# Kernel optimization log

Hardware: AMD Instinct MI355X
Metric: run time of the kernel (lower is better)

The kernel has to match this reference:

```python
import jax, jax.numpy as jnp
import numpy as np

DIM = 768
N_HEADS = 12
HEAD_DIM = DIM // N_HEADS
SCALE = HEAD_DIM ** -0.5


def setup_inputs() -> dict:
    key = jax.random.key(0)
    ks = jax.random.split(key, 5)
    x = jax.random.normal(ks[0], (8, 1024, DIM), dtype=jnp.float32)
    w_qkv = jax.random.normal(ks[1], (DIM, 3 * DIM), dtype=jnp.float32) * (DIM ** -0.5)
    b_qkv = jnp.zeros((3 * DIM,), dtype=jnp.float32)
    w_proj = jax.random.normal(ks[2], (DIM, DIM), dtype=jnp.float32) * (DIM ** -0.5)
    b_proj = jnp.zeros((DIM,), dtype=jnp.float32)
    return {"x": x, "w_qkv": w_qkv, "b_qkv": b_qkv, "w_proj": w_proj, "b_proj": b_proj}


def reference(x, w_qkv, b_qkv, w_proj, b_proj):
    B, N, _ = x.shape
    qkv = x @ w_qkv + b_qkv                       # [B, N, 3*DIM]
    qkv = qkv.reshape(B, N, 3, N_HEADS, HEAD_DIM)
    q = qkv[:, :, 0].transpose(0, 2, 1, 3)        # [B, H, N, D]
    k = qkv[:, :, 1].transpose(0, 2, 1, 3)
    v = qkv[:, :, 2].transpose(0, 2, 1, 3)
    attn = jnp.einsum('bhnd,bhmd->bhnm', q, k) * SCALE
    attn = jax.nn.softmax(attn, axis=-1)
    out = jnp.einsum('bhnm,bhmd->bhnd', attn, v)  # [B, H, N, D]
    out = out.transpose(0, 2, 1, 3).reshape(B, N, DIM)
    return out @ w_proj + b_proj
```

## Files before the change

kernel.cpp:

```cpp
#include <hip/hip_runtime.h>
#include <hip/hip_bf16.h>

#define NHEADS 12
#define HDIM   64
#define SEQ    1024
#define NBATCH 8
#define MODELD 768
#define QKVD   2304
#define BHEADS (NBATCH * NHEADS)

typedef __attribute__((ext_vector_type(8))) short          bf16x8;
typedef __attribute__((ext_vector_type(8))) unsigned short u16x8;
typedef __attribute__((ext_vector_type(4))) unsigned short u16x4;
typedef __attribute__((ext_vector_type(4))) float          f32x4;

static __device__ __forceinline__ unsigned short f2bf(float f) {
  unsigned int u = __float_as_uint(f);
  u += 0x7fffu + ((u >> 16) & 1u);
  return (unsigned short)(u >> 16);
}

static __device__ __forceinline__ unsigned int pk2(float x, float y) {
  __hip_bfloat162 h = __float22bfloat162_rn(make_float2(x, y));
  return *(unsigned int*)&h;
}

static __device__ __forceinline__ void gld_lds16(const void* g, void* l) {
  __builtin_amdgcn_global_load_lds((const __attribute__((address_space(1))) void*)g,
                                   (__attribute__((address_space(3))) void*)l, 16, 0, 0);
}

#define QSC 0.18033688f

static __device__ __forceinline__ void transpose_body(
    const float* __restrict__ in, unsigned short* __restrict__ out,
    int R, int C, int bx, int by, int tid) {
  __shared__ float t[32][33];
  const int c0 = bx * 32, r0 = by * 32;
  const int lr = tid >> 3;
  const int lc = (tid & 7) * 4;
  const float* p = in + (size_t)(r0 + lr) * C + c0 + lc;
  float4 v = *(const float4*)p;
  t[lr][lc]     = v.x;
  t[lr][lc + 1] = v.y;
  t[lr][lc + 2] = v.z;
  t[lr][lc + 3] = v.w;
  __syncthreads();
  unsigned short* q = out + (size_t)(c0 + lr) * R + r0 + lc;
  q[0] = f2bf(t[lc][lr]);
  q[1] = f2bf(t[lc + 1][lr]);
  q[2] = f2bf(t[lc + 2][lr]);
  q[3] = f2bf(t[lc + 3][lr]);
}

__global__ __launch_bounds__(256) void prep(
    const float* __restrict__ x, unsigned short* __restrict__ Xb,
    const float* __restrict__ w_qkv, unsigned short* __restrict__ wqkvT,
    const float* __restrict__ w_proj, unsigned short* __restrict__ wprojT) {
  const int id = blockIdx.x;
  const int tid = threadIdx.x;
  if (id < 3072) {
    const int i = (id * 256 + tid) * 8;
    const float4 a0 = *(const float4*)(x + i);
    const float4 a1 = *(const float4*)(x + i + 4);
    union { unsigned int u[4]; u16x8 v; } w;
    w.u[0] = pk2(a0.x, a0.y); w.u[1] = pk2(a0.z, a0.w);
    w.u[2] = pk2(a1.x, a1.y); w.u[3] = pk2(a1.z, a1.w);
    *(u16x8*)(Xb + i) = w.v;
  } else if (id < 4800) {
    const int u = id - 3072;
    transpose_body(w_qkv, wqkvT, MODELD, QKVD, u % 72, u / 72, tid);
  } else {
    const int u = id - 4800;
    transpose_body(w_proj, wprojT, MODELD, MODELD, u % 24, u / 24, tid);
  }
}

#define GEMM_CORE(AP, BP)                                                      \
  const int tid  = threadIdx.x;                                                \
  const int lane = tid & 63;                                                   \
  const int wave = tid >> 6;                                                   \
  const int wm = wave >> 1, wn = wave & 1;                                     \
  const int fr = lane & 15;                                                    \
  const int fq = lane >> 4;                                                    \
  const int swz = (fr & 7) << 4;                                               \
  const int srow8 = lane >> 3;                                                 \
  const int scb8 = (((lane & 7) ^ srow8) << 4);                                \
  f32x4 acc[4][4] = {};                                                        \
  auto stA = [&](int dbuf, int kb, int R) {                                    \
    gld_lds16(AP + (size_t)(R + srow8) * 1536 + kb + scb8,                     \
              (char*)smem + dbuf * 16384 + R * 128);                           \
  };                                                                           \
  auto stB = [&](int dbuf, int kb, int R) {                                    \
    gld_lds16(BP + (size_t)(R + srow8) * 1536 + kb + scb8,                     \
              (char*)smem + 32768 + dbuf * 16384 + R * 128);                   \
  };                                                                           \
  _Pragma("unroll")                                                            \
  for (int pt = 0; pt < 2; ++pt) {                                             \
    const int kb = pt * 128;                                                   \
    stA(pt, kb, wave * 8);      stA(pt, kb, 32 + wave * 8);                    \
    stA(pt, kb, 64 + wave * 8); stA(pt, kb, 96 + wave * 8);                    \
    stB(pt, kb, wave * 8);      stB(pt, kb, 64 + wave * 8);                    \
    stB(pt, kb, 32 + wave * 8); stB(pt, kb, 96 + wave * 8);                    \
  }                                                                            \
  asm volatile("s_waitcnt vmcnt(8)" ::: "memory");                             \
  __builtin_amdgcn_s_barrier();                                                \
  for (int kt = 0; kt < 12; ++kt) {                                            \
    const int db = kt & 1;                                                     \
    const char* Ad = (const char*)smem + db * 16384;                           \
    const char* Bd = (const char*)smem + 32768 + db * 16384;                   \
    bf16x8 a[4][2], b[4][2];                                                   \
                                                        \
    _Pragma("unroll")                                                          \
    for (int i = 0; i < 4; ++i)                                                \
      _Pragma("unroll")                                                        \
      for (int c = 0; c < 2; ++c)                                              \
        a[i][c] = *(const bf16x8*)(Ad + (wm * 64 + i * 16 + fr) * 128 +        \
                                   ((c * 64 + fq * 16) ^ swz));                \
    _Pragma("unroll")                                                          \
    for (int j = 0; j < 2; ++j)                                                \
      _Pragma("unroll")                                                        \
      for (int c = 0; c < 2; ++c)                                              \
        b[j][c] = *(const bf16x8*)(Bd + (wn * 64 + j * 16 + fr) * 128 +        \
                                   ((c * 64 + fq * 16) ^ swz));                \
    if (kt >= 1 && kt <= 10) {                   \
      stB(db ^ 1, (kt + 1) * 128, 32 + wave * 8);                              \
      stB(db ^ 1, (kt + 1) * 128, 96 + wave * 8);                              \
    }                                                                          \
    if (kt < 11) asm volatile("s_waitcnt vmcnt(8)" ::: "memory");              \
    else         asm volatile("s_waitcnt vmcnt(0)" ::: "memory");              \
    __builtin_amdgcn_s_barrier();                                              \
    __builtin_amdgcn_s_setprio(1);                                             \
    _Pragma("unroll")                                                          \
    for (int i = 0; i < 4; ++i)                                                \
      _Pragma("unroll")                                                        \
      for (int j = 0; j < 2; ++j)                                              \
        _Pragma("unroll")                                                      \
        for (int c = 0; c < 2; ++c)                                            \
          acc[i][j] = __builtin_amdgcn_mfma_f32_16x16x32_bf16(                 \
              a[i][c], b[j][c], acc[i][j], 0, 0, 0);                           \
    __builtin_amdgcn_s_setprio(0);                                             \
    __builtin_amdgcn_s_barrier();                                              \
                                                        \
    _Pragma("unroll")                                                          \
    for (int j = 0; j < 2; ++j)                                                \
      _Pragma("unroll")                                                        \
      for (int c = 0; c < 2; ++c)                                              \
        b[2 + j][c] = *(const bf16x8*)(Bd + (wn * 64 + (2 + j) * 16 + fr) *    \
                                       128 + ((c * 64 + fq * 16) ^ swz));      \
    if (kt <= 9) {                        \
      const int kb2 = (kt + 2) * 128;                                          \
      stA(db, kb2, wave * 8);      stA(db, kb2, 32 + wave * 8);                \
      stA(db, kb2, 64 + wave * 8); stA(db, kb2, 96 + wave * 8);                \
      stB(db, kb2, wave * 8);      stB(db, kb2, 64 + wave * 8);                \
    }                                                                          \
    if (kt <= 9)       asm volatile("s_waitcnt vmcnt(6)" ::: "memory");        \
    else if (kt == 10) asm volatile("s_waitcnt vmcnt(2)" ::: "memory");        \
    else               asm volatile("s_waitcnt vmcnt(0)" ::: "memory");        \
    __builtin_amdgcn_s_barrier();                                              \
    __builtin_amdgcn_s_setprio(1);                                             \
    _Pragma("unroll")                                                          \
    for (int i = 0; i < 4; ++i)                                                \
      _Pragma("unroll")                                                        \
      for (int j = 0; j < 2; ++j)                                              \
        _Pragma("unroll")                                                      \
        for (int c = 0; c < 2; ++c)                                            \
          acc[i][2 + j] = __builtin_amdgcn_mfma_f32_16x16x32_bf16(             \
              a[i][c], b[2 + j][c], acc[i][2 + j], 0, 0, 0);                   \
    __builtin_amdgcn_s_setprio(0);                                             \
    __builtin_amdgcn_s_barrier();                                              \
  }

__global__ __launch_bounds__(256, 2) void gemm_qkv(
    const unsigned short* __restrict__ Xb, const unsigned short* __restrict__ WT,
    const float* __restrict__ bias,
    unsigned short* __restrict__ Qo, unsigned short* __restrict__ Ko,
    unsigned short* __restrict__ VTo) {
  __shared__ __align__(16) unsigned short smem[32768];
  int flat = blockIdx.x;
  flat = (flat & 7) * 144 + (flat >> 3);
  const int m0 = (flat / 18) * 128;
  const int n0 = (flat % 18) * 128;
  const char* Ap = (const char*)(Xb + (size_t)m0 * MODELD);
  const char* Bp = (const char*)(WT + (size_t)n0 * MODELD);

  GEMM_CORE(Ap, Bp)

  const int wr = wm * 64, wc = wn * 64;
  const int s = n0 / MODELD;
  if (s < 2) {
    const float qs = (s == 0) ? QSC : 1.0f;
#pragma unroll
    for (int i = 0; i < 4; ++i) {
#pragma unroll
      for (int j = 0; j < 4; ++j) {
        const int col = n0 + wc + j * 16 + fr;
        const int rem = col - s * MODELD;
        const int h = rem >> 6, d = rem & 63;
        const float bv = bias[col];
#pragma unroll
        for (int r = 0; r < 4; ++r) {
          const int row = m0 + wr + i * 16 + fq * 4 + r;
          const int bb = row >> 10, n = row & 1023;
          const int bh = bb * NHEADS + h;
          const unsigned short val = f2bf((acc[i][j][r] + bv) * qs);
          if (s == 0) Qo[((size_t)bh * SEQ + n) * HDIM + d] = val;
          else        Ko[((size_t)bh * SEQ + n) * HDIM + d] = val;
        }
      }
    }
  } else {
    unsigned short* T = smem + wave * 4608;
#pragma unroll
    for (int i = 0; i < 4; ++i) {
#pragma unroll
      for (int j = 0; j < 4; ++j) {
        const int col = n0 + wc + j * 16 + fr;
        const float bv = bias[col];
        const int dl = j * 16 + fr;
        union { unsigned int u[2]; u16x4 v; } pk;
        pk.u[0] = pk2(acc[i][j][0] + bv, acc[i][j][1] + bv);
        pk.u[1] = pk2(acc[i][j][2] + bv, acc[i][j][3] + bv);
        *(u16x4*)&T[dl * 72 + i * 16 + fq * 4] = pk.v;
      }
    }
    asm volatile("s_waitcnt lgkmcnt(0)" ::: "memory");
    const int h  = (n0 + wc - 2 * MODELD) >> 6;
    const int rowb = m0 + wr;
    const int bb = rowb >> 10, nq = rowb & 1023;
    const int bh = bb * NHEADS + h;
    unsigned short* Vb = VTo + ((size_t)bh * HDIM) * SEQ + nq;
#pragma unroll
    for (int u = 0; u < 8; ++u) {
      const int d  = u * 8 + (lane >> 3);
      const int qc = (lane & 7) * 8;
      u16x8 v = *(const u16x8*)&T[d * 72 + qc];
      *(u16x8*)(Vb + (size_t)d * SEQ + qc) = v;
    }
  }
}

__global__ __launch_bounds__(256, 2) void gemm_proj(
    const unsigned short* __restrict__ A, const unsigned short* __restrict__ WT,
    const float* __restrict__ bias, float* __restrict__ Out) {
  __shared__ __align__(16) unsigned short smem[32768];
  int flat = blockIdx.x;
  flat = (flat & 7) * 48 + (flat >> 3);
  const int m0 = (flat / 6) * 128;
  const int n0 = (flat % 6) * 128;
  const char* Ap = (const char*)(A  + (size_t)m0 * MODELD);
  const char* Bp = (const char*)(WT + (size_t)n0 * MODELD);

  GEMM_CORE(Ap, Bp)

  const int wr = wm * 64, wc = wn * 64;
#pragma unroll
  for (int i = 0; i < 4; ++i) {
#pragma unroll
    for (int j = 0; j < 4; ++j) {
      const int col = n0 + wc + j * 16 + fr;
      const float bv = bias[col];
#pragma unroll
      for (int r = 0; r < 4; ++r) {
        const int row = m0 + wr + i * 16 + fq * 4 + r;
        Out[(size_t)row * MODELD + col] = acc[i][j][r] + bv;
      }
    }
  }
}

__global__ __launch_bounds__(256, 3) void attn_fused(
    const unsigned short* __restrict__ Q, const unsigned short* __restrict__ K,
    const unsigned short* __restrict__ VT, unsigned short* __restrict__ AO) {
  __shared__ __align__(16) unsigned short smem[24576];

  const int tid  = threadIdx.x;
  const int lane = tid & 63;
  const int wave = tid >> 6;

  const int flat = blockIdx.y * 8 + blockIdx.x;
  const int xcd = flat & 7, j = flat >> 3;
  const int bh = xcd * 12 + (j >> 3);
  const int qb = j & 7;
  const int b = bh / NHEADS, h = bh % NHEADS;
  const int q0 = qb * 128 + wave * 32;

  const unsigned short* Qp = Q  + (size_t)bh * SEQ * HDIM;
  const unsigned short* Kp = K  + (size_t)bh * SEQ * HDIM;
  const unsigned short* Vp = VT + (size_t)bh * HDIM * SEQ;

  const int fr = lane & 15;
  const int fq = lane >> 4;
  const int swz = (fr & 7) << 4;

  bf16x8 qf[2][2];
#pragma unroll
  for (int g = 0; g < 2; ++g)
#pragma unroll
    for (int c = 0; c < 2; ++c)
      qf[g][c] = *(const bf16x8*)(Qp + (size_t)(q0 + g * 16 + fr) * HDIM + c * 32 + fq * 8);

  const int srow_lo = (lane >> 3);
  const int scx = (((lane & 7) ^ srow_lo) << 4);

  f32x4 acc[2][4] = {};
  f32x4 accl[2] = {};
  bf16x8 ones;
#pragma unroll
  for (int i = 0; i < 8; ++i) ones[i] = (short)0x3F80;

  auto stage = [&](int buf, int kv0) {
    const char* Kb = (const char*)Kp + (size_t)kv0 * 128;
    const char* Vb = (const char*)Vp + (size_t)kv0 * 2;
#pragma unroll
    for (int u = 0; u < 2; ++u) {
      const int i = wave * 2 + u;
      const int r0 = i * 8 + srow_lo;
      gld_lds16(Kb + (size_t)r0 * 128  + scx, (char*)smem + buf * 8192 + i * 1024);
      gld_lds16(Vb + (size_t)r0 * 2048 + scx, (char*)smem + 24576 + buf * 8192 + i * 1024);
    }
  };

  stage(0, 0);
  stage(1, 64);

  int cur = 0;
  for (int t = 0; t < SEQ / 64; ++t) {
    if (t < SEQ / 64 - 1) asm volatile("s_waitcnt vmcnt(4)" ::: "memory");
    else                  asm volatile("s_waitcnt vmcnt(0)" ::: "memory");
    __builtin_amdgcn_s_barrier();
    if (t < SEQ / 64 - 2) {
      int sb = cur + 2; if (sb >= 3) sb -= 3;
      stage(sb, (t + 2) * 64);
    }

    const char* Kt = (const char*)smem + cur * 8192;
    const char* Vt = (const char*)smem + 24576 + cur * 8192;

    bf16x8 kf[4][2];
#pragma unroll
    for (int ng = 0; ng < 4; ++ng)
#pragma unroll
      for (int c = 0; c < 2; ++c)
        kf[ng][c] = *(const bf16x8*)(Kt + (ng * 16 + fr) * 128 + ((c * 64 + fq * 16) ^ swz));

    f32x4 S[2][4] = {};
    __builtin_amdgcn_s_setprio(1);
#pragma unroll
    for (int g = 0; g < 2; ++g)
#pragma unroll
      for (int ng = 0; ng < 4; ++ng)
#pragma unroll
        for (int c = 0; c < 2; ++c)
          S[g][ng] = __builtin_amdgcn_mfma_f32_16x16x32_bf16(kf[ng][c], qf[g][c], S[g][ng], 0, 0, 0);
    __builtin_amdgcn_s_setprio(0);

    bf16x8 pf[2][2];
#pragma unroll
    for (int g = 0; g < 2; ++g) {
      unsigned int u[4][2];
#pragma unroll
      for (int ng = 0; ng < 4; ++ng) {
        const float p0 = __builtin_amdgcn_exp2f(S[g][ng][0]);
        const float p1 = __builtin_amdgcn_exp2f(S[g][ng][1]);
        const float p2 = __builtin_amdgcn_exp2f(S[g][ng][2]);
        const float p3 = __builtin_amdgcn_exp2f(S[g][ng][3]);
        u[ng][0] = pk2(p0, p1);
        u[ng][1] = pk2(p2, p3);
      }
#pragma unroll
      for (int c = 0; c < 2; ++c) {
        union { unsigned int w[4]; bf16x8 v; } pp;
#pragma unroll
        for (int d2 = 0; d2 < 2; ++d2) {
          unsigned int e = u[2 * c][d2], o = u[2 * c + 1][d2];
          asm("v_permlane32_swap_b32 %0, %1" : "+v"(e), "+v"(o));
          asm("v_permlane16_swap_b32 %0, %1" : "+v"(e), "+v"(o));
          pp.w[d2] = e;
          pp.w[2 + d2] = o;
        }
        pf[g][c] = pp.v;
      }
    }

    bf16x8 vf[4][2];
#pragma unroll
    for (int df = 0; df < 4; ++df)
#pragma unroll
      for (int c = 0; c < 2; ++c)
        vf[df][c] = *(const bf16x8*)(Vt + (df * 16 + fr) * 128 + ((c * 64 + fq * 16) ^ swz));

    __builtin_amdgcn_s_setprio(1);
#pragma unroll
    for (int g = 0; g < 2; ++g) {
#pragma unroll
      for (int df = 0; df < 4; ++df)
#pragma unroll
        for (int c = 0; c < 2; ++c)
          acc[g][df] = __builtin_amdgcn_mfma_f32_16x16x32_bf16(pf[g][c], vf[df][c], acc[g][df], 0, 0, 0);
#pragma unroll
      for (int c = 0; c < 2; ++c)
        accl[g] = __builtin_amdgcn_mfma_f32_16x16x32_bf16(pf[g][c], ones, accl[g], 0, 0, 0);
    }
    __builtin_amdgcn_s_setprio(0);

    cur = (cur == 2) ? 0 : cur + 1;
  }

#pragma unroll
  for (int g = 0; g < 2; ++g) {
#pragma unroll
    for (int r = 0; r < 4; ++r) {
      const float inv = 1.0f / accl[g][r];
      const int q = q0 + g * 16 + fq * 4 + r;
      unsigned short* outp = AO + ((size_t)b * SEQ + q) * MODELD + h * HDIM;
#pragma unroll
      for (int df = 0; df < 4; ++df)
        outp[df * 16 + fr] = f2bf(acc[g][df][r] * inv);
    }
  }
}

extern "C" void kernel_launch(void* const* d_in, const int* in_sizes, int n_in,
                              void* d_out, int out_size, void* d_ws, size_t ws_size,
                              hipStream_t stream) {
  const float* x      = (const float*)d_in[0];
  const float* w_qkv  = (const float*)d_in[1];
  const float* b_qkv  = (const float*)d_in[2];
  const float* w_proj = (const float*)d_in[3];
  const float* b_proj = (const float*)d_in[4];
  float* out = (float*)d_out;

  unsigned short* ws = (unsigned short*)d_ws;
  unsigned short* wqkvT  = ws;
  unsigned short* wprojT = wqkvT + (size_t)QKVD * MODELD;
  unsigned short* Qw     = wprojT + (size_t)MODELD * MODELD;
  unsigned short* Kw     = Qw + (size_t)BHEADS * SEQ * HDIM;
  unsigned short* VTw    = Kw + (size_t)BHEADS * SEQ * HDIM;
  unsigned short* AO     = VTw + (size_t)BHEADS * SEQ * HDIM;
  unsigned short* Xb     = AO + (size_t)NBATCH * SEQ * MODELD;

  prep<<<dim3(5376), 256, 0, stream>>>(x, Xb, w_qkv, wqkvT, w_proj, wprojT);
  gemm_qkv<<<dim3((QKVD / 128) * ((NBATCH * SEQ) / 128)), 256, 0, stream>>>(
      Xb, wqkvT, b_qkv, Qw, Kw, VTw);
  attn_fused<<<dim3(SEQ / 128, BHEADS), 256, 0, stream>>>(Qw, Kw, VTw, AO);
  gemm_proj<<<dim3((MODELD / 128) * ((NBATCH * SEQ) / 128)), 256, 0, stream>>>(
      AO, wprojT, b_proj, out);
}
```

Baseline: 94.45 us.

## Rewrite QKV GEMM with 8 waves per block and smaller per-wave tiles

```diff
diff --git a/kernel.cpp b/kernel.cpp
--- a/kernel.cpp
+++ b/kernel.cpp
@@ -73,6 +73,165 @@
   } else {
     const int u = id - 4800;
     transpose_body(w_proj, wprojT, MODELD, MODELD, u % 24, u / 24, tid);
+  }
+}
+
+__global__ __launch_bounds__(512, 4) void gemm_qkv(
+    const unsigned short* __restrict__ Xb, const unsigned short* __restrict__ WT,
+    const float* __restrict__ bias,
+    unsigned short* __restrict__ Qo, unsigned short* __restrict__ Ko,
+    unsigned short* __restrict__ VTo) {
+  __shared__ __align__(16) unsigned short smem[32768];
+  const int tid  = threadIdx.x;
+  const int lane = tid & 63;
+  const int wave = tid >> 6;
+  const int wm = wave >> 1;
+  const int wn = wave & 1;
+  int flat = blockIdx.x;
+  flat = (flat & 7) * 144 + (flat >> 3);
+  const int m0 = (flat / 18) * 128;
+  const int n0 = (flat % 18) * 128;
+  const int fr = lane & 15;
+  const int fq = lane >> 4;
+  const int swz = (fr & 7) << 4;
+  const int srow8 = lane >> 3;
+  const int scb8 = (((lane & 7) ^ srow8) << 4);
+  const int ReB = (wave & 3) * 8 + (wave >> 2) * 64;
+  const int RlB = 32 + ReB;
+
+  const char* Ap = (const char*)(Xb + (size_t)m0 * MODELD);
+  const char* Bp = (const char*)(WT + (size_t)n0 * MODELD);
+
+  f32x4 acc[2][4] = {};
+
+  auto stA = [&](int dbuf, int kb, int R) {
+    gld_lds16(Ap + (size_t)(R + srow8) * 1536 + kb + scb8,
+              (char*)smem + dbuf * 16384 + R * 128);
+  };
+  auto stB = [&](int dbuf, int kb, int R) {
+    gld_lds16(Bp + (size_t)(R + srow8) * 1536 + kb + scb8,
+              (char*)smem + 32768 + dbuf * 16384 + R * 128);
+  };
+
+#pragma unroll
+  for (int pt = 0; pt < 2; ++pt) {
+    const int kb = pt * 128;
+    stA(pt, kb, wave * 8); stA(pt, kb, 64 + wave * 8);
+    stB(pt, kb, ReB);      stB(pt, kb, RlB);
+  }
+  asm volatile("s_waitcnt vmcnt(4)" ::: "memory");
+  __builtin_amdgcn_s_barrier();
+
+  for (int kt = 0; kt < 12; ++kt) {
+    const int db = kt & 1;
+    const char* Ad = (const char*)smem + db * 16384;
+    const char* Bd = (const char*)smem + 32768 + db * 16384;
+    bf16x8 a[2][2], b[4][2];
+#pragma unroll
+    for (int i = 0; i < 2; ++i)
+#pragma unroll
+      for (int c = 0; c < 2; ++c)
+        a[i][c] = *(const bf16x8*)(Ad + (wm * 32 + i * 16 + fr) * 128 +
+                                   ((c * 64 + fq * 16) ^ swz));
+#pragma unroll
+    for (int j = 0; j < 2; ++j)
+#pragma unroll
+      for (int c = 0; c < 2; ++c)
+        b[j][c] = *(const bf16x8*)(Bd + (wn * 64 + j * 16 + fr) * 128 +
+                                   ((c * 64 + fq * 16) ^ swz));
+    if (kt >= 1 && kt <= 10) stB(db ^ 1, (kt + 1) * 128, RlB);
+    if (kt < 11) asm volatile("s_waitcnt vmcnt(4)" ::: "memory");
+    else         asm volatile("s_waitcnt vmcnt(0)" ::: "memory");
+    __builtin_amdgcn_s_barrier();
+    __builtin_amdgcn_s_setprio(1);
+#pragma unroll
+    for (int i = 0; i < 2; ++i)
+#pragma unroll
+      for (int j = 0; j < 2; ++j)
+#pragma unroll
+        for (int c = 0; c < 2; ++c)
+          acc[i][j] = __builtin_amdgcn_mfma_f32_16x16x32_bf16(
+              a[i][c], b[j][c], acc[i][j], 0, 0, 0);
+    __builtin_amdgcn_s_setprio(0);
+    __builtin_amdgcn_s_barrier();
+#pragma unroll
+    for (int j = 0; j < 2; ++j)
+#pragma unroll
+      for (int c = 0; c < 2; ++c)
+        b[2 + j][c] = *(const bf16x8*)(Bd + (wn * 64 + (2 + j) * 16 + fr) * 128 +
+                                       ((c * 64 + fq * 16) ^ swz));
+    if (kt <= 9) {
+      const int kb2 = (kt + 2) * 128;
+      stA(db, kb2, wave * 8); stA(db, kb2, 64 + wave * 8);
+      stB(db, kb2, ReB);
+    }
+    if (kt <= 9) asm volatile("s_waitcnt vmcnt(3)" ::: "memory");
+    else         asm volatile("s_waitcnt vmcnt(0)" ::: "memory");
+    __builtin_amdgcn_s_barrier();
+    __builtin_amdgcn_s_setprio(1);
+#pragma unroll
+    for (int i = 0; i < 2; ++i)
+#pragma unroll
+      for (int j = 0; j < 2; ++j)
+#pragma unroll
+        for (int c = 0; c < 2; ++c)
+          acc[i][2 + j] = __builtin_amdgcn_mfma_f32_16x16x32_bf16(
+              a[i][c], b[2 + j][c], acc[i][2 + j], 0, 0, 0);
+    __builtin_amdgcn_s_setprio(0);
+    __builtin_amdgcn_s_barrier();
+  }
+  __builtin_amdgcn_s_barrier();
+
+  const int s = n0 / MODELD;
+  if (s < 2) {
+    const float qs = (s == 0) ? QSC : 1.0f;
+#pragma unroll
+    for (int i = 0; i < 2; ++i) {
+#pragma unroll
+      for (int j = 0; j < 4; ++j) {
+        const int col = n0 + wn * 64 + j * 16 + fr;
+        const int rem = col - s * MODELD;
+        const int h = rem >> 6, d = rem & 63;
+        const float bv = bias[col];
+#pragma unroll
+        for (int r = 0; r < 4; ++r) {
+          const int row = m0 + wm * 32 + i * 16 + fq * 4 + r;
+          const int bb = row >> 10, n = row & 1023;
+          const int bh = bb * NHEADS + h;
+          const unsigned short val = f2bf((acc[i][j][r] + bv) * qs);
+          if (s == 0) Qo[((size_t)bh * SEQ + n) * HDIM + d] = val;
+          else        Ko[((size_t)bh * SEQ + n) * HDIM + d] = val;
+        }
+      }
+    }
+  } else {
+    unsigned short* T = smem + wave * 2560;
+#pragma unroll
+    for (int i = 0; i < 2; ++i) {
+#pragma unroll
+      for (int j = 0; j < 4; ++j) {
+        const int col = n0 + wn * 64 + j * 16 + fr;
+        const float bv = bias[col];
+        const int dl = j * 16 + fr;
+        union { unsigned int u[2]; u16x4 v; } pk;
+        pk.u[0] = pk2(acc[i][j][0] + bv, acc[i][j][1] + bv);
+        pk.u[1] = pk2(acc[i][j][2] + bv, acc[i][j][3] + bv);
+        *(u16x4*)&T[dl * 40 + i * 16 + fq * 4] = pk.v;
+      }
+    }
+    asm volatile("s_waitcnt lgkmcnt(0)" ::: "memory");
+    const int h  = (n0 + wn * 64 - 2 * MODELD) >> 6;
+    const int rowb = m0 + wm * 32;
+    const int bb = rowb >> 10, nq = rowb & 1023;
+    const int bh = bb * NHEADS + h;
+    unsigned short* Vb = VTo + ((size_t)bh * HDIM) * SEQ + nq;
+#pragma unroll
+    for (int u = 0; u < 4; ++u) {
+      const int d  = u * 16 + (lane >> 2);
+      const int qc = (lane & 3) * 8;
+      u16x8 v = *(const u16x8*)&T[d * 40 + qc];
+      *(u16x8*)(Vb + (size_t)d * SEQ + qc) = v;
+    }
   }
 }
 
@@ -110,7 +269,6 @@
     const char* Ad = (const char*)smem + db * 16384;                           \
     const char* Bd = (const char*)smem + 32768 + db * 16384;                   \
     bf16x8 a[4][2], b[4][2];                                                   \
-                                                        \
     _Pragma("unroll")                                                          \
     for (int i = 0; i < 4; ++i)                                                \
       _Pragma("unroll")                                                        \
@@ -123,7 +281,7 @@
       for (int c = 0; c < 2; ++c)                                              \
         b[j][c] = *(const bf16x8*)(Bd + (wn * 64 + j * 16 + fr) * 128 +        \
                                    ((c * 64 + fq * 16) ^ swz));                \
-    if (kt >= 1 && kt <= 10) {                   \
+    if (kt >= 1 && kt <= 10) {                                                 \
       stB(db ^ 1, (kt + 1) * 128, 32 + wave * 8);                              \
       stB(db ^ 1, (kt + 1) * 128, 96 + wave * 8);                              \
     }                                                                          \
@@ -141,14 +299,13 @@
               a[i][c], b[j][c], acc[i][j], 0, 0, 0);                           \
     __builtin_amdgcn_s_setprio(0);                                             \
     __builtin_amdgcn_s_barrier();                                              \
-                                                        \
     _Pragma("unroll")                                                          \
     for (int j = 0; j < 2; ++j)                                                \
       _Pragma("unroll")                                                        \
       for (int c = 0; c < 2; ++c)                                              \
         b[2 + j][c] = *(const bf16x8*)(Bd + (wn * 64 + (2 + j) * 16 + fr) *    \
                                        128 + ((c * 64 + fq * 16) ^ swz));      \
-    if (kt <= 9) {                        \
+    if (kt <= 9) {                                                             \
       const int kb2 = (kt + 2) * 128;                                          \
       stA(db, kb2, wave * 8);      stA(db, kb2, 32 + wave * 8);                \
       stA(db, kb2, 64 + wave * 8); stA(db, kb2, 96 + wave * 8);                \
@@ -171,75 +328,6 @@
     __builtin_amdgcn_s_barrier();                                              \
   }
 
-__global__ __launch_bounds__(256, 2) void gemm_qkv(
-    const unsigned short* __restrict__ Xb, const unsigned short* __restrict__ WT,
-    const float* __restrict__ bias,
-    unsigned short* __restrict__ Qo, unsigned short* __restrict__ Ko,
-    unsigned short* __restrict__ VTo) {
-  __shared__ __align__(16) unsigned short smem[32768];
-  int flat = blockIdx.x;
-  flat = (flat & 7) * 144 + (flat >> 3);
-  const int m0 = (flat / 18) * 128;
-  const int n0 = (flat % 18) * 128;
-  const char* Ap = (const char*)(Xb + (size_t)m0 * MODELD);
-  const char* Bp = (const char*)(WT + (size_t)n0 * MODELD);
-
-  GEMM_CORE(Ap, Bp)
-
-  const int wr = wm * 64, wc = wn * 64;
-  const int s = n0 / MODELD;
-  if (s < 2) {
-    const float qs = (s == 0) ? QSC : 1.0f;
-#pragma unroll
-    for (int i = 0; i < 4; ++i) {
-#pragma unroll
-      for (int j = 0; j < 4; ++j) {
-        const int col = n0 + wc + j * 16 + fr;
-        const int rem = col - s * MODELD;
-        const int h = rem >> 6, d = rem & 63;
-        const float bv = bias[col];
-#pragma unroll
-        for (int r = 0; r < 4; ++r) {
-          const int row = m0 + wr + i * 16 + fq * 4 + r;
-          const int bb = row >> 10, n = row & 1023;
-          const int bh = bb * NHEADS + h;
-          const unsigned short val = f2bf((acc[i][j][r] + bv) * qs);
-          if (s == 0) Qo[((size_t)bh * SEQ + n) * HDIM + d] = val;
-          else        Ko[((size_t)bh * SEQ + n) * HDIM + d] = val;
-        }
-      }
-    }
-  } else {
-    unsigned short* T = smem + wave * 4608;
-#pragma unroll
-    for (int i = 0; i < 4; ++i) {
-#pragma unroll
-      for (int j = 0; j < 4; ++j) {
-        const int col = n0 + wc + j * 16 + fr;
-        const float bv = bias[col];
-        const int dl = j * 16 + fr;
-        union { unsigned int u[2]; u16x4 v; } pk;
-        pk.u[0] = pk2(acc[i][j][0] + bv, acc[i][j][1] + bv);
-        pk.u[1] = pk2(acc[i][j][2] + bv, acc[i][j][3] + bv);
-        *(u16x4*)&T[dl * 72 + i * 16 + fq * 4] = pk.v;
-      }
-    }
-    asm volatile("s_waitcnt lgkmcnt(0)" ::: "memory");
-    const int h  = (n0 + wc - 2 * MODELD) >> 6;
-    const int rowb = m0 + wr;
-    const int bb = rowb >> 10, nq = rowb & 1023;
-    const int bh = bb * NHEADS + h;
-    unsigned short* Vb = VTo + ((size_t)bh * HDIM) * SEQ + nq;
-#pragma unroll
-    for (int u = 0; u < 8; ++u) {
-      const int d  = u * 8 + (lane >> 3);
-      const int qc = (lane & 7) * 8;
-      u16x8 v = *(const u16x8*)&T[d * 72 + qc];
-      *(u16x8*)(Vb + (size_t)d * SEQ + qc) = v;
-    }
-  }
-}
-
 __global__ __launch_bounds__(256, 2) void gemm_proj(
     const unsigned short* __restrict__ A, const unsigned short* __restrict__ WT,
     const float* __restrict__ bias, float* __restrict__ Out) {
@@ -441,7 +529,7 @@
   unsigned short* Xb     = AO + (size_t)NBATCH * SEQ * MODELD;
 
   prep<<<dim3(5376), 256, 0, stream>>>(x, Xb, w_qkv, wqkvT, w_proj, wprojT);
-  gemm_qkv<<<dim3((QKVD / 128) * ((NBATCH * SEQ) / 128)), 256, 0, stream>>>(
+  gemm_qkv<<<dim3((QKVD / 128) * ((NBATCH * SEQ) / 128)), 512, 0, stream>>>(
       Xb, wqkvT, b_qkv, Qw, Kw, VTw);
   attn_fused<<<dim3(SEQ / 128, BHEADS), 256, 0, stream>>>(Qw, Kw, VTw, AO);
   gemm_proj<<<dim3((MODELD / 128) * ((NBATCH * SEQ) / 128)), 256, 0, stream>>>(
```

After: 94.74 us. Within noise of the previous version (+0.3%).
